# Kernel tuning notes

Measured on AMD Instinct MI355X. Metric: run time of the kernel, lower is better.

## Reference

```python
import jax, jax.numpy as jnp
import numpy as np

B, N = 8, 2048
D_MODEL, D_QK, NHEAD, N_K, D_FF = 256, 128, 8, 16, 1024
LN_EPS = 1e-5


def _layer_norm(x, g, b):
    m = jnp.mean(x, axis=-1, keepdims=True)
    v = jnp.var(x, axis=-1, keepdims=True)
    return (x - m) * jax.lax.rsqrt(v + LN_EPS) * g + b


def _l2_normalize(x):
    # F.normalize(dim=-1): x / max(||x||_2, 1e-12)
    n = jnp.sqrt(jnp.sum(x * x, axis=-1, keepdims=True))
    return x / jnp.maximum(n, 1e-12)


def setup_inputs() -> dict:
    key = jax.random.key(0)
    ks = jax.random.split(key, 12)
    s = 0.02
    return {
        "x": jax.random.normal(ks[0], (B, N, D_MODEL), dtype=jnp.float32),
        # linear_q / linear_k (d_model -> d_model_qk)
        "Wq": jax.random.normal(ks[1], (D_MODEL, D_QK), dtype=jnp.float32) * s,
        "bq": jnp.zeros((D_QK,), jnp.float32),
        "Wk": jax.random.normal(ks[2], (D_MODEL, D_QK), dtype=jnp.float32) * s,
        "bk": jnp.zeros((D_QK,), jnp.float32),
        # NoLinearQKMHA: value + output projections (d_model -> d_model)
        "Wv": jax.random.normal(ks[3], (D_MODEL, D_MODEL), dtype=jnp.float32) * s,
        "bv": jnp.zeros((D_MODEL,), jnp.float32),
        "Wo": jax.random.normal(ks[4], (D_MODEL, D_MODEL), dtype=jnp.float32) * s,
        "bo": jnp.zeros((D_MODEL,), jnp.float32),
        # norm1 (applied to gathered values)
        "g1": jnp.ones((D_MODEL,), jnp.float32),
        "b1": jnp.zeros((D_MODEL,), jnp.float32),
        # ffn: LayerNorm -> Linear -> GELU -> Linear
        "gf": jnp.ones((D_MODEL,), jnp.float32),
        "bf": jnp.zeros((D_MODEL,), jnp.float32),
        "W1": jax.random.normal(ks[5], (D_MODEL, D_FF), dtype=jnp.float32) * s,
        "b1f": jnp.zeros((D_FF,), jnp.float32),
        "W2": jax.random.normal(ks[6], (D_FF, D_MODEL), dtype=jnp.float32) * s,
        "b2f": jnp.zeros((D_MODEL,), jnp.float32),
        # residual_weight (init 0 in torch; nonzero here for a meaningful baseline)
        "rw": jnp.full((1,), 0.5, jnp.float32),
    }


def reference(x, Wq, bq, Wk, bk, Wv, bv, Wo, bo, g1, b1, gf, bf, W1, b1f, W2, b2f, rw):
    # --- project + normalize queries/keys ---
    qn = _l2_normalize(x @ Wq + bq)   # [B,N,Dqk]
    kn = _l2_normalize(x @ Wk + bk)   # [B,N,Dqk]

    # --- KNN: k smallest Euclidean distances from each query to keys ---
    d2 = (jnp.sum(qn * qn, -1)[:, :, None]
          + jnp.sum(kn * kn, -1)[:, None, :]
          - 2.0 * jnp.einsum('bqd,bkd->bqk', qn, kn))   # [B,N,N]
    _, idx = jax.lax.top_k(-d2, N_K)                     # [B,N,n_k]

    # --- gather neighbors ---
    gather = jax.vmap(lambda arr, ind: arr[ind])
    x_v = gather(x, idx)    # [B,N,n_k,D_MODEL]
    x_k = gather(kn, idx)   # [B,N,n_k,Dqk]

    # --- windowed MHA (NoLinearQK: q,k used directly; v projected) ---
    xnorm = _layer_norm(x_v, g1, b1)
    v = xnorm @ Wv + bv                                  # [B,N,n_k,D_MODEL]
    dh, dv = D_QK // NHEAD, D_MODEL // NHEAD
    qh = qn.reshape(B, N, NHEAD, dh)
    kh = x_k.reshape(B, N, N_K, NHEAD, dh)
    vh = v.reshape(B, N, N_K, NHEAD, dv)
    logits = jnp.einsum('bnhd,bnkhd->bnhk', qh, kh) / np.float32(np.sqrt(dh))
    attn = jax.nn.softmax(logits, axis=-1)
    o = jnp.einsum('bnhk,bnkhe->bnhe', attn, vh).reshape(B, N, D_MODEL)
    o = o @ Wo + bo

    # --- residuals (eval: dropout = identity) ---
    x = x + o * rw
    h = _layer_norm(x, gf, bf) @ W1 + b1f
    h = jax.nn.gelu(h, approximate=False) @ W2 + b2f
    x = x + h * rw
    return x
```

## Files before the change

### kernel.cpp

```cpp
#include <hip/hip_runtime.h>
#include <math.h>

#define BATCH 8
#define SEQ   2048
#define DM    256
#define DQK   128
#define NHEADS 8
#define NK    16
#define DFF   1024

typedef __attribute__((ext_vector_type(8))) short short8;
typedef __attribute__((ext_vector_type(8))) _Float16 half8;
typedef __attribute__((ext_vector_type(4))) float floatx4;
typedef unsigned long long ull;

__device__ __forceinline__ unsigned short f2bf(float f) {
    unsigned int u = __float_as_uint(f);
    u += 0x7fffu + ((u >> 16) & 1u);
    return (unsigned short)(u >> 16);
}

__device__ __forceinline__ float gelu_fast(float h) {
    float y = 0.7978845608028654f * (h + 0.044715f * h * h * h);
    float e = __expf(2.f * y);
    float t = 1.f - 2.f / (e + 1.f);
    return 0.5f * h * (1.f + t);
}

__device__ __forceinline__ ull mkkey(float f, int gidx) {
    unsigned int u = __float_as_uint(f);
    u ^= (unsigned int)((int)u >> 31) | 0x80000000u;
    return ((ull)u << 32) | (unsigned int)(2047 - gidx);
}

__device__ __forceinline__ ull shfl_xor_u64(ull v, int m) {
    unsigned int lo = (unsigned int)v, hi = (unsigned int)(v >> 32);
    lo = __shfl_xor(lo, m);
    hi = __shfl_xor(hi, m);
    return ((ull)hi << 32) | lo;
}

__global__ __launch_bounds__(256) void conv_kernel(
    const float* __restrict__ W1, const float* __restrict__ W2,
    const float* __restrict__ Wv, const float* __restrict__ Wo,
    unsigned short* __restrict__ W1f, unsigned short* __restrict__ W2f,
    unsigned short* __restrict__ Wvf, unsigned short* __restrict__ Wof)
{
    int g = blockIdx.x * 256 + threadIdx.x;
    const float* W; unsigned short* O; int e, stride;
    if (g < 32768)      { W = W1; O = W1f; e = g;         stride = DFF; }
    else if (g < 65536) { W = W2; O = W2f; e = g - 32768; stride = DM;  }
    else if (g < 73728) { W = Wv; O = Wvf; e = g - 65536; stride = DM;  }
    else                { W = Wo; O = Wof; e = g - 73728; stride = DM;  }
    int lane = e & 63;
    int kk, nt;
    if (g < 32768)      { kk = (e >> 6) & 7;  nt = e >> 9;  }
    else if (g < 65536) { kk = (e >> 6) & 31; nt = e >> 11; }
    else                { kk = (e >> 6) & 7;  nt = e >> 9;  }
    int n = nt * 16 + (lane & 15);
    int k0 = kk * 32 + (lane >> 4) * 8;
    unsigned int pk[4];
    #pragma unroll
    for (int jj = 0; jj < 4; ++jj) {
        unsigned short lo = f2bf(W[(size_t)(k0 + 2 * jj) * stride + n]);
        unsigned short hi = f2bf(W[(size_t)(k0 + 2 * jj + 1) * stride + n]);
        pk[jj] = (unsigned int)lo | ((unsigned int)hi << 16);
    }
    *(uint4*)(O + (size_t)e * 8) = make_uint4(pk[0], pk[1], pk[2], pk[3]);
}

__global__ __launch_bounds__(256) void proj_qk_kernel(
    const float* __restrict__ x,
    const float* __restrict__ Wq, const float* __restrict__ bq,
    const float* __restrict__ Wk, const float* __restrict__ bk,
    float* __restrict__ qn, float* __restrict__ kn,
    unsigned short* __restrict__ knTh, unsigned short* __restrict__ knTl,
    float* __restrict__ knsq)
{
    __shared__ __align__(16) float xs[8 * 256];
    __shared__ __align__(16) float ks[8 * 128];
    __shared__ float nred[8][2], kred[8][2], k2red[8][2];

    const int tid = threadIdx.x;
    const int b = blockIdx.x & 7;
    const int chunk = blockIdx.x >> 3;
    const size_t t0 = (size_t)b * SEQ + (size_t)chunk * 8;

    for (int i = tid; i < 8 * 256; i += 256) xs[i] = x[t0 * DM + i];
    __syncthreads();

    {
        const int col = tid & 127, half = tid >> 7;
        float qa[4] = {0.f, 0.f, 0.f, 0.f}, ka[4] = {0.f, 0.f, 0.f, 0.f};
        for (int d = 0; d < 256; ++d) {
            float wq = Wq[d * DQK + col];
            float wk = Wk[d * DQK + col];
            #pragma unroll
            for (int t = 0; t < 4; ++t) {
                float xv = xs[(half * 4 + t) * 256 + d];
                qa[t] = fmaf(xv, wq, qa[t]);
                ka[t] = fmaf(xv, wk, ka[t]);
            }
        }
        #pragma unroll
        for (int t = 0; t < 4; ++t) { qa[t] += bq[col]; ka[t] += bk[col]; }

        const int sub = (tid >> 6) & 1;
        #pragma unroll
        for (int t = 0; t < 4; ++t) {
            float sq = qa[t] * qa[t], sk = ka[t] * ka[t];
            #pragma unroll
            for (int m = 1; m < 64; m <<= 1) { sq += __shfl_xor(sq, m); sk += __shfl_xor(sk, m); }
            if ((tid & 63) == 0) { nred[half * 4 + t][sub] = sq; kred[half * 4 + t][sub] = sk; }
        }
        __syncthreads();
        float kvv[4];
        #pragma unroll
        for (int t = 0; t < 4; ++t) {
            int tok = half * 4 + t;
            float nq = sqrtf(nred[tok][0] + nred[tok][1]);
            float nk = sqrtf(kred[tok][0] + kred[tok][1]);
            float qv = qa[t] / fmaxf(nq, 1e-12f);
            float kv = ka[t] / fmaxf(nk, 1e-12f);
            qn[(t0 + tok) * DQK + col] = qv;
            kn[(t0 + tok) * DQK + col] = kv;
            ks[tok * 128 + col] = kv;
            kvv[t] = kv;
        }
        #pragma unroll
        for (int t = 0; t < 4; ++t) {
            float s2 = kvv[t] * kvv[t];
            #pragma unroll
            for (int m = 1; m < 64; m <<= 1) s2 += __shfl_xor(s2, m);
            if ((tid & 63) == 0) k2red[half * 4 + t][sub] = s2;
        }
        __syncthreads();
        if (tid < 8) knsq[t0 + tid] = k2red[tid][0] + k2red[tid][1];
    }

    {
        const int e   = tid & 127;
        const int sel = tid >> 7;
        const int key = e & 7;
        const int kq  = e >> 3;
        const int kk  = kq >> 2, qd = kq & 3;
        const int nt  = chunk >> 1;
        const int n   = ((chunk & 1) << 3) + key;
        const float* src = &ks[key * 128 + kk * 32 + qd * 8];
        unsigned int pk[4];
        #pragma unroll
        for (int jj = 0; jj < 4; ++jj) {
            float v0 = src[2 * jj], v1 = src[2 * jj + 1];
            _Float16 h0 = (_Float16)v0, h1 = (_Float16)v1;
            unsigned short u0, u1;
            if (sel == 0) {
                u0 = __builtin_bit_cast(unsigned short, h0);
                u1 = __builtin_bit_cast(unsigned short, h1);
            } else {
                _Float16 l0 = (_Float16)((v0 - (float)h0) * 4096.f);
                _Float16 l1 = (_Float16)((v1 - (float)h1) * 4096.f);
                u0 = __builtin_bit_cast(unsigned short, l0);
                u1 = __builtin_bit_cast(unsigned short, l1);
            }
            pk[jj] = (unsigned int)u0 | ((unsigned int)u1 << 16);
        }
        unsigned short* dst = (sel ? knTl : knTh)
            + (size_t)b * 262144
            + (size_t)((nt * 4 + kk) * 64 + qd * 16 + n) * 8;
        *(uint4*)dst = make_uint4(pk[0], pk[1], pk[2], pk[3]);
    }
}

__global__ __launch_bounds__(256) void proj_v_kernel(
    const float* __restrict__ x,
    const float* __restrict__ bv, const float* __restrict__ g1,
    const float* __restrict__ b1,
    const unsigned short* __restrict__ Wvf, float* __restrict__ vall)
{
    __shared__ __align__(16) float xs[16][260];
    __shared__ float stat_m[16], stat_r[16];
    __shared__ float bvs[256], g1s[256], b1s[256];

    const int tid = threadIdx.x;
    const int lane = tid & 63, wave = tid >> 6;
    const int quad = lane >> 4, lr = lane & 15;
    const size_t t0 = (size_t)blockIdx.x * 16;

    for (int i = tid; i < 16 * 256; i += 256) xs[i >> 8][i & 255] = x[t0 * DM + i];
    bvs[tid] = bv[tid]; g1s[tid] = g1[tid]; b1s[tid] = b1[tid];
    __syncthreads();

    {
        int tok = tid >> 4, l = tid & 15;
        float s = 0.f, s2 = 0.f;
        #pragma unroll
        for (int i = 0; i < 16; ++i) {
            float v = xs[tok][l + 16 * i];
            s += v; s2 += v * v;
        }
        #pragma unroll
        for (int m = 1; m < 16; m <<= 1) { s += __shfl_xor(s, m); s2 += __shfl_xor(s2, m); }
        if (l == 0) {
            float mean = s * (1.f / 256.f);
            float var  = s2 * (1.f / 256.f) - mean * mean;
            stat_m[tok] = mean;
            stat_r[tok] = rsqrtf(var + 1e-5f);
        }
    }
    __syncthreads();

    short8 av[8];
    {
        float mm = stat_m[lr], rr = stat_r[lr];
        #pragma unroll
        for (int kk = 0; kk < 8; ++kk) {
            #pragma unroll
            for (int j = 0; j < 8; ++j) {
                int k = kk * 32 + quad * 8 + j;
                float v = (xs[lr][k] - mm) * rr * g1s[k] + b1s[k];
                av[kk][j] = (short)f2bf(v);
            }
        }
    }
    floatx4 acc[4];
    #pragma unroll
    for (int nt = 0; nt < 4; ++nt) acc[nt] = (floatx4){0.f, 0.f, 0.f, 0.f};
    #pragma unroll
    for (int nt = 0; nt < 4; ++nt) {
        #pragma unroll
        for (int kk = 0; kk < 8; ++kk) {
            short8 bfr = *(const short8*)(Wvf + ((size_t)(((wave * 4 + nt) * 8 + kk) * 64) + lane) * 8);
            acc[nt] = __builtin_amdgcn_mfma_f32_16x16x32_bf16(av[kk], bfr, acc[nt], 0, 0, 0);
        }
    }
    #pragma unroll
    for (int nt = 0; nt < 4; ++nt) {
        int col = (wave * 4 + nt) * 16 + lr;
        float bb = bvs[col];
        #pragma unroll
        for (int reg = 0; reg < 4; ++reg) {
            int row = quad * 4 + reg;
            vall[(t0 + row) * DM + col] = acc[nt][reg] + bb;
        }
    }
}

__global__ __launch_bounds__(256, 4) void attn_kernel(
    const float* __restrict__ x,
    const float* __restrict__ qn_g, const float* __restrict__ kn_g,
    const unsigned short* __restrict__ knTh, const unsigned short* __restrict__ knTl,
    const float* __restrict__ knsq_g,
    const float* __restrict__ vall,
    const unsigned short* __restrict__ Wof, const float* __restrict__ bo,
    const float* __restrict__ rw, float* __restrict__ out)
{
    __shared__ __align__(16) float s_ld[8 * 1024];
    __shared__ __align__(16) float qs[8 * DQK];
    __shared__ ull candK[8][32];
    __shared__ int topidx[8 * NK];
    float* attn_s = s_ld;
    float* o8     = s_ld + 1024;

    const int tid = threadIdx.x;
    const int lane = tid & 63, wave = tid >> 6;
    const int quad = lane >> 4, lr = lane & 15;
    const int sg = lane >> 5, sl = lane & 31;
    const int qsel = wave * 2 + sg;
    const int b = blockIdx.x & 7;
    const int chunk = blockIdx.x >> 3;
    const size_t tq0 = (size_t)b * SEQ + (size_t)chunk * 8;
    const size_t rowb = (size_t)b * SEQ;

    *(float4*)&qs[tid * 4] = *(const float4*)&qn_g[tq0 * DQK + tid * 4];

    half8 a_hi[4], a_lo[4];
    {
        const float* qrow = qn_g + (tq0 + (lr & 7)) * DQK + quad * 8;
        #pragma unroll
        for (int kk = 0; kk < 4; ++kk) {
            float4 fa = *(const float4*)(qrow + kk * 32);
            float4 fb = *(const float4*)(qrow + kk * 32 + 4);
            float vv[8] = {fa.x, fa.y, fa.z, fa.w, fb.x, fb.y, fb.z, fb.w};
            #pragma unroll
            for (int j = 0; j < 8; ++j) {
                float v = vv[j];
                _Float16 h = (_Float16)v;
                a_hi[kk][j] = h;
                a_lo[kk][j] = (_Float16)((v - (float)h) * 4096.f);
            }
        }
    }
    __syncthreads();

    const unsigned short* bh = knTh + (size_t)b * 262144;
    const unsigned short* bl = knTl + (size_t)b * 262144;
    const float* ksqb = knsq_g + rowb;

    for (int h = 0; h < 2; ++h) {
        if (h) __syncthreads();

        for (int t = 0; t < 16; ++t) {
            const int tile = h * 64 + wave * 16 + t;
            const unsigned short* ph = bh + (size_t)tile * 2048 + lane * 8;
            const unsigned short* pl = bl + (size_t)tile * 2048 + lane * 8;
            floatx4 am  = (floatx4){0.f, 0.f, 0.f, 0.f};
            floatx4 ax1 = (floatx4){0.f, 0.f, 0.f, 0.f};
            floatx4 ax2 = (floatx4){0.f, 0.f, 0.f, 0.f};
            #pragma unroll
            for (int kk = 0; kk < 4; ++kk) {
                half8 bhf = *(const half8*)(ph + kk * 512);
                half8 blf = *(const half8*)(pl + kk * 512);
                am  = __builtin_amdgcn_mfma_f32_16x16x32_f16(a_hi[kk], bhf, am,  0, 0, 0);
                ax1 = __builtin_amdgcn_mfma_f32_16x16x32_f16(a_hi[kk], blf, ax1, 0, 0, 0);
                ax2 = __builtin_amdgcn_mfma_f32_16x16x32_f16(a_lo[kk], bhf, ax2, 0, 0, 0);
            }
            if (lane < 32) {
                const int keyloc = (wave * 16 + t) * 16 + lr;
                const float kq = ksqb[h * 1024 + keyloc];
                #pragma unroll
                for (int r = 0; r < 4; ++r) {
                    s_ld[(quad * 4 + r) * 1024 + keyloc] =
                        2.f * (am[r] + (ax1[r] + ax2[r]) * (1.f / 4096.f)) - kq;
                }
            }
        }
        __syncthreads();

        {
            const float* srow = &s_ld[qsel * 1024 + sl];
            float f0 = -INFINITY, f1 = -INFINITY;
            int   i0 = 0, i1 = 0;
            #pragma unroll
            for (int i = 0; i < 32; ++i) {
                float f = srow[32 * i];
                int gidx = h * 1024 + sl + 32 * i;
                bool a  = f > f0;
                bool bb = f > f1;
                f1 = a ? f0 : (bb ? f    : f1);
                i1 = a ? i0 : (bb ? gidx : i1);
                f0 = a ? f    : f0;
                i0 = a ? gidx : i0;
            }
            ull k2v = mkkey(f1, i1);
            ull cur = mkkey(f0, i0);
            int cnt = 0;
            for (int r = 0; r < NK; ++r) {
                ull w = cur;
                #pragma unroll
                for (int m = 1; m < 32; m <<= 1) {
                    ull o = shfl_xor_u64(w, m);
                    if (o > w) w = o;
                }
                if (sl == 0) candK[qsel][h * 16 + r] = w;
                if (cur == w) {
                    ++cnt;
                    if (cnt == 1) cur = k2v;
                    else {
                        ull best = 0;
                        #pragma unroll
                        for (int i = 0; i < 32; ++i) {
                            float f = srow[32 * i];
                            ull k = mkkey(f, h * 1024 + sl + 32 * i);
                            if (k < w && k > best) best = k;
                        }
                        cur = best;
                    }
                }
            }
        }
    }
    __syncthreads();

    {
        ull cur = candK[qsel][sl];
        for (int r = 0; r < NK; ++r) {
            ull w = cur;
            #pragma unroll
            for (int m = 1; m < 32; m <<= 1) {
                ull o = shfl_xor_u64(w, m);
                if (o > w) w = o;
            }
            if (sl == 0) topidx[qsel * NK + r] = 2047 - (int)(unsigned int)(w & 0xFFFFFFFFull);
            if (cur == w) cur = 0;
        }
    }
    __syncthreads();

    for (int qq = 0; qq < 2; ++qq) {
        const int q = wave + 4 * qq;
        const int h = lane >> 3;
        const int k1 = lane & 7, k2 = 8 + (lane & 7);
        const int i1 = topidx[q * NK + k1], i2 = topidx[q * NK + k2];
        const float* kr1 = kn_g + (rowb + i1) * DQK + h * 16;
        const float* kr2 = kn_g + (rowb + i2) * DQK + h * 16;
        float lg1 = 0.f, lg2 = 0.f;
        #pragma unroll
        for (int d = 0; d < 16; d += 4) {
            float4 qv = *(const float4*)&qs[q * DQK + h * 16 + d];
            float4 a1 = *(const float4*)&kr1[d];
            float4 a2 = *(const float4*)&kr2[d];
            lg1 = fmaf(qv.x, a1.x, lg1); lg1 = fmaf(qv.y, a1.y, lg1);
            lg1 = fmaf(qv.z, a1.z, lg1); lg1 = fmaf(qv.w, a1.w, lg1);
            lg2 = fmaf(qv.x, a2.x, lg2); lg2 = fmaf(qv.y, a2.y, lg2);
            lg2 = fmaf(qv.z, a2.z, lg2); lg2 = fmaf(qv.w, a2.w, lg2);
        }
        lg1 *= 0.25f; lg2 *= 0.25f;
        float mx = fmaxf(lg1, lg2);
        #pragma unroll
        for (int m = 1; m < 8; m <<= 1) mx = fmaxf(mx, __shfl_xor(mx, m));
        float e1 = expf(lg1 - mx), e2 = expf(lg2 - mx);
        float ssum = e1 + e2;
        #pragma unroll
        for (int m = 1; m < 8; m <<= 1) ssum += __shfl_xor(ssum, m);
        attn_s[q * 128 + h * 16 + k1] = e1 / ssum;
        attn_s[q * 128 + h * 16 + k2] = e2 / ssum;
        __syncthreads();

        float o[4] = {0.f, 0.f, 0.f, 0.f};
        for (int k = 0; k < NK; ++k) {
            const float* vr = vall + (rowb + topidx[q * NK + k]) * DM;
            #pragma unroll
            for (int j = 0; j < 4; ++j) {
                int d = lane + 64 * j;
                o[j] = fmaf(attn_s[q * 128 + (d >> 5) * 16 + k], vr[d], o[j]);
            }
        }
        #pragma unroll
        for (int j = 0; j < 4; ++j) o8[q * 260 + lane + 64 * j] = o[j];
        __syncthreads();
    }

    {
        short8 ao[8];
        #pragma unroll
        for (int kk = 0; kk < 8; ++kk) {
            #pragma unroll
            for (int j = 0; j < 8; ++j) {
                int k = kk * 32 + quad * 8 + j;
                float v = (lr < 8) ? o8[lr * 260 + k] : 0.f;
                ao[kk][j] = (short)f2bf(v);
            }
        }
        floatx4 aw[4];
        #pragma unroll
        for (int nt = 0; nt < 4; ++nt) aw[nt] = (floatx4){0.f, 0.f, 0.f, 0.f};
        #pragma unroll
        for (int nt = 0; nt < 4; ++nt) {
            #pragma unroll
            for (int kk = 0; kk < 8; ++kk) {
                short8 bofr = *(const short8*)(Wof + ((size_t)(((wave * 4 + nt) * 8 + kk) * 64) + lane) * 8);
                aw[nt] = __builtin_amdgcn_mfma_f32_16x16x32_bf16(ao[kk], bofr, aw[nt], 0, 0, 0);
            }
        }
        float rwv = rw[0];
        if (quad < 2) {
            #pragma unroll
            for (int nt = 0; nt < 4; ++nt) {
                int col = (wave * 4 + nt) * 16 + lr;
                float bov = bo[col];
                #pragma unroll
                for (int reg = 0; reg < 4; ++reg) {
                    int row = quad * 4 + reg;
                    size_t t = tq0 + row;
                    out[t * DM + col] = x[t * DM + col] + (aw[nt][reg] + bov) * rwv;
                }
            }
        }
    }
}

__global__ __launch_bounds__(256, 2) void ffn_kernel(
    float* __restrict__ io,
    const float* __restrict__ gf, const float* __restrict__ bf,
    const unsigned short* __restrict__ W1f, const float* __restrict__ b1f,
    const unsigned short* __restrict__ W2f, const float* __restrict__ b2f,
    const float* __restrict__ rw)
{
    __shared__ __align__(16) float xs[16][260];
    __shared__ float gfs[256], bfs[256], b2s[256], b1s[1024];
    __shared__ float stat_m[16], stat_r[16];
    __shared__ __align__(16) unsigned short Af[8 * 64 * 8];
    __shared__ __align__(16) unsigned short G[16][1032];

    const int tid = threadIdx.x;
    const int lane = tid & 63, wave = tid >> 6;
    const int quad = lane >> 4, lr = lane & 15;
    const size_t t0 = (size_t)blockIdx.x * 16;

    for (int i = tid; i < 16 * 256; i += 256) xs[i >> 8][i & 255] = io[t0 * DM + i];
    gfs[tid] = gf[tid]; bfs[tid] = bf[tid]; b2s[tid] = b2f[tid];
    for (int i = tid; i < 1024; i += 256) b1s[i] = b1f[i];
    __syncthreads();

    {
        int tok = tid >> 4, l = tid & 15;
        float s = 0.f, s2 = 0.f;
        #pragma unroll
        for (int i = 0; i < 16; ++i) {
            float v = xs[tok][l + 16 * i];
            s += v; s2 += v * v;
        }
        #pragma unroll
        for (int m = 1; m < 16; m <<= 1) { s += __shfl_xor(s, m); s2 += __shfl_xor(s2, m); }
        if (l == 0) {
            float mean = s * (1.f / 256.f);
            float var  = s2 * (1.f / 256.f) - mean * mean;
            stat_m[tok] = mean;
            stat_r[tok] = rsqrtf(var + 1e-5f);
        }
    }
    __syncthreads();

    for (int kk = wave; kk < 8; kk += 4) {
        int m = lr, k0 = kk * 32 + quad * 8;
        float mm = stat_m[m], rr = stat_r[m];
        unsigned int pk[4];
        #pragma unroll
        for (int jj = 0; jj < 4; ++jj) {
            int ka = k0 + 2 * jj, kb = ka + 1;
            float v0 = (xs[m][ka] - mm) * rr * gfs[ka] + bfs[ka];
            float v1 = (xs[m][kb] - mm) * rr * gfs[kb] + bfs[kb];
            pk[jj] = (unsigned int)f2bf(v0) | ((unsigned int)f2bf(v1) << 16);
        }
        *(uint4*)&Af[(kk * 64 + lane) * 8] = make_uint4(pk[0], pk[1], pk[2], pk[3]);
    }
    __syncthreads();

    short8 afr[8];
    #pragma unroll
    for (int kk = 0; kk < 8; ++kk)
        afr[kk] = *(const short8*)&Af[(kk * 64 + lane) * 8];

    floatx4 acc[16];
    #pragma unroll
    for (int nt = 0; nt < 16; ++nt) acc[nt] = (floatx4){0.f, 0.f, 0.f, 0.f};

    const unsigned short* w1p = W1f + ((size_t)(wave * 16) * 8 * 64) * 8;
    for (int nt = 0; nt < 16; ++nt) {
        #pragma unroll
        for (int kk = 0; kk < 8; ++kk) {
            short8 bfr = *(const short8*)(w1p + (size_t)((nt * 8 + kk) * 64 + lane) * 8);
            acc[nt] = __builtin_amdgcn_mfma_f32_16x16x32_bf16(afr[kk], bfr, acc[nt], 0, 0, 0);
        }
    }

    #pragma unroll
    for (int nt = 0; nt < 16; ++nt) {
        #pragma unroll
        for (int reg = 0; reg < 4; ++reg) {
            int n = wave * 256 + nt * 16 + lr;
            int row = quad * 4 + reg;
            float h = acc[nt][reg] + b1s[n];
            G[row][n] = f2bf(gelu_fast(h));
        }
    }
    __syncthreads();

    floatx4 acc2[4];
    #pragma unroll
    for (int nt = 0; nt < 4; ++nt) acc2[nt] = (floatx4){0.f, 0.f, 0.f, 0.f};

    for (int kk2 = 0; kk2 < 32; ++kk2) {
        short8 a2 = *(const short8*)&G[lr][kk2 * 32 + quad * 8];
        #pragma unroll
        for (int nt = 0; nt < 4; ++nt) {
            short8 b2 = *(const short8*)(W2f + (size_t)(((wave * 4 + nt) * 32 + kk2) * 64 + lane) * 8);
            acc2[nt] = __builtin_amdgcn_mfma_f32_16x16x32_bf16(a2, b2, acc2[nt], 0, 0, 0);
        }
    }

    float rwv = rw[0];
    #pragma unroll
    for (int nt = 0; nt < 4; ++nt) {
        #pragma unroll
        for (int reg = 0; reg < 4; ++reg) {
            int col = wave * 64 + nt * 16 + lr;
            int row = quad * 4 + reg;
            float o = acc2[nt][reg] + b2s[col];
            io[(t0 + row) * DM + col] = xs[row][col] + o * rwv;
        }
    }
}

extern "C" void kernel_launch(void* const* d_in, const int* in_sizes, int n_in,
                              void* d_out, int out_size, void* d_ws, size_t ws_size,
                              hipStream_t stream)
{
    const float* x   = (const float*)d_in[0];
    const float* Wq  = (const float*)d_in[1];
    const float* bq  = (const float*)d_in[2];
    const float* Wk  = (const float*)d_in[3];
    const float* bk  = (const float*)d_in[4];
    const float* Wv  = (const float*)d_in[5];
    const float* bv  = (const float*)d_in[6];
    const float* Wo  = (const float*)d_in[7];
    const float* bo  = (const float*)d_in[8];
    const float* g1  = (const float*)d_in[9];
    const float* b1  = (const float*)d_in[10];
    const float* gf  = (const float*)d_in[11];
    const float* bf  = (const float*)d_in[12];
    const float* W1  = (const float*)d_in[13];
    const float* b1f = (const float*)d_in[14];
    const float* W2  = (const float*)d_in[15];
    const float* b2f = (const float*)d_in[16];
    const float* rw  = (const float*)d_in[17];
    float* out = (float*)d_out;

    float* ws   = (float*)d_ws;
    float* qn   = ws;
    float* kn   = ws + 2097152;
    unsigned short* knTh = (unsigned short*)(ws + 4194304);
    unsigned short* knTl = knTh + 2097152;
    float* vall = ws + 6291456;
    float* knsq = ws + 10485760;
    unsigned short* W1f = (unsigned short*)(ws + 10502144);
    unsigned short* W2f = W1f + 262144;
    unsigned short* Wvf = W2f + 262144;
    unsigned short* Wof = Wvf + 65536;

    conv_kernel<<<320, 256, 0, stream>>>(W1, W2, Wv, Wo, W1f, W2f, Wvf, Wof);
    proj_qk_kernel<<<BATCH * SEQ / 8, 256, 0, stream>>>(x, Wq, bq, Wk, bk,
                                                        qn, kn, knTh, knTl, knsq);
    proj_v_kernel<<<BATCH * SEQ / 16, 256, 0, stream>>>(x, bv, g1, b1, Wvf, vall);
    attn_kernel<<<BATCH * SEQ / 8, 256, 0, stream>>>(x, qn, kn, knTh, knTl, knsq, vall,
                                                     Wof, bo, rw, out);
    ffn_kernel<<<BATCH * SEQ / 16, 256, 0, stream>>>(out, gf, bf, W1f, b1f, W2f, b2f, rw);
}
```

Before: 381.3 us.

## Process 16 queries per attention block and 32 tokens per FFN block

The attention kernel now handles 16 queries per block instead of 8. This fills all 16 MFMA rows, which were previously half wasted, so each key tile read from memory serves twice as many queries. The top-k stage is restructured into four key quarters with candidates held in registers, and the final merge uses the two candidates per lane. The FFN kernel moves to 512 threads and 32 tokens per block so each W1/W2 fragment feeds two row tiles. The cost is fewer blocks, more LDS per block, and higher register pressure.

```diff
diff --git a/kernel.cpp b/kernel.cpp
--- a/kernel.cpp
+++ b/kernel.cpp
@@ -254,28 +254,24 @@
     const unsigned short* __restrict__ Wof, const float* __restrict__ bo,
     const float* __restrict__ rw, float* __restrict__ out)
 {
-    __shared__ __align__(16) float s_ld[8 * 1024];
-    __shared__ __align__(16) float qs[8 * DQK];
-    __shared__ ull candK[8][32];
-    __shared__ int topidx[8 * NK];
+    __shared__ __align__(16) float s_ld[16 * 512];
+    __shared__ int topidx[16 * NK];
     float* attn_s = s_ld;
-    float* o8     = s_ld + 1024;
+    float* o8     = s_ld + 2048;
 
     const int tid = threadIdx.x;
     const int lane = tid & 63, wave = tid >> 6;
     const int quad = lane >> 4, lr = lane & 15;
     const int sg = lane >> 5, sl = lane & 31;
-    const int qsel = wave * 2 + sg;
+    const int sgid = wave * 2 + sg;
     const int b = blockIdx.x & 7;
     const int chunk = blockIdx.x >> 3;
-    const size_t tq0 = (size_t)b * SEQ + (size_t)chunk * 8;
+    const size_t tq0 = (size_t)b * SEQ + (size_t)chunk * 16;
     const size_t rowb = (size_t)b * SEQ;
 
-    *(float4*)&qs[tid * 4] = *(const float4*)&qn_g[tq0 * DQK + tid * 4];
-
     half8 a_hi[4], a_lo[4];
     {
-        const float* qrow = qn_g + (tq0 + (lr & 7)) * DQK + quad * 8;
+        const float* qrow = qn_g + (tq0 + lr) * DQK + quad * 8;
         #pragma unroll
         for (int kk = 0; kk < 4; ++kk) {
             float4 fa = *(const float4*)(qrow + kk * 32);
@@ -290,17 +286,18 @@
             }
         }
     }
-    __syncthreads();
 
     const unsigned short* bh = knTh + (size_t)b * 262144;
     const unsigned short* bl = knTl + (size_t)b * 262144;
     const float* ksqb = knsq_g + rowb;
 
-    for (int h = 0; h < 2; ++h) {
-        if (h) __syncthreads();
-
-        for (int t = 0; t < 16; ++t) {
-            const int tile = h * 64 + wave * 16 + t;
+    ull c0[2], c1[2];
+
+    for (int q4 = 0; q4 < 4; ++q4) {
+        if (q4) __syncthreads();
+
+        for (int t = 0; t < 8; ++t) {
+            const int tile = q4 * 32 + wave * 8 + t;
             const unsigned short* ph = bh + (size_t)tile * 2048 + lane * 8;
             const unsigned short* pl = bl + (size_t)tile * 2048 + lane * 8;
             floatx4 am  = (floatx4){0.f, 0.f, 0.f, 0.f};
@@ -314,26 +311,26 @@
                 ax1 = __builtin_amdgcn_mfma_f32_16x16x32_f16(a_hi[kk], blf, ax1, 0, 0, 0);
                 ax2 = __builtin_amdgcn_mfma_f32_16x16x32_f16(a_lo[kk], bhf, ax2, 0, 0, 0);
             }
-            if (lane < 32) {
-                const int keyloc = (wave * 16 + t) * 16 + lr;
-                const float kq = ksqb[h * 1024 + keyloc];
-                #pragma unroll
-                for (int r = 0; r < 4; ++r) {
-                    s_ld[(quad * 4 + r) * 1024 + keyloc] =
-                        2.f * (am[r] + (ax1[r] + ax2[r]) * (1.f / 4096.f)) - kq;
-                }
+            const int keyloc = (wave * 8 + t) * 16 + lr;
+            const float kq = ksqb[q4 * 512 + keyloc];
+            #pragma unroll
+            for (int r = 0; r < 4; ++r) {
+                s_ld[(quad * 4 + r) * 512 + keyloc] =
+                    2.f * (am[r] + (ax1[r] + ax2[r]) * (1.f / 4096.f)) - kq;
             }
         }
         __syncthreads();
 
-        {
-            const float* srow = &s_ld[qsel * 1024 + sl];
+        #pragma unroll
+        for (int qi = 0; qi < 2; ++qi) {
+            const int q = sgid + 8 * qi;
+            const float* srow = &s_ld[q * 512 + sl];
             float f0 = -INFINITY, f1 = -INFINITY;
             int   i0 = 0, i1 = 0;
             #pragma unroll
-            for (int i = 0; i < 32; ++i) {
+            for (int i = 0; i < 16; ++i) {
                 float f = srow[32 * i];
-                int gidx = h * 1024 + sl + 32 * i;
+                int gidx = q4 * 512 + sl + 32 * i;
                 bool a  = f > f0;
                 bool bb = f > f1;
                 f1 = a ? f0 : (bb ? f    : f1);
@@ -351,16 +348,18 @@
                     ull o = shfl_xor_u64(w, m);
                     if (o > w) w = o;
                 }
-                if (sl == 0) candK[qsel][h * 16 + r] = w;
+                const int slot = q4 * 16 + r;
+                if (sl == slot)      c0[qi] = w;
+                if (sl == slot - 32) c1[qi] = w;
                 if (cur == w) {
                     ++cnt;
                     if (cnt == 1) cur = k2v;
                     else {
                         ull best = 0;
                         #pragma unroll
-                        for (int i = 0; i < 32; ++i) {
+                        for (int i = 0; i < 16; ++i) {
                             float f = srow[32 * i];
-                            ull k = mkkey(f, h * 1024 + sl + 32 * i);
+                            ull k = mkkey(f, q4 * 512 + sl + 32 * i);
                             if (k < w && k > best) best = k;
                         }
                         cur = best;
@@ -371,8 +370,14 @@
     }
     __syncthreads();
 
-    {
-        ull cur = candK[qsel][sl];
+    #pragma unroll
+    for (int qi = 0; qi < 2; ++qi) {
+        const int q = sgid + 8 * qi;
+        ull ca = c0[qi], cb = c1[qi];
+        ull hi = ca > cb ? ca : cb;
+        ull lo = ca > cb ? cb : ca;
+        ull cur = hi;
+        int cnt = 0;
         for (int r = 0; r < NK; ++r) {
             ull w = cur;
             #pragma unroll
@@ -380,23 +385,24 @@
                 ull o = shfl_xor_u64(w, m);
                 if (o > w) w = o;
             }
-            if (sl == 0) topidx[qsel * NK + r] = 2047 - (int)(unsigned int)(w & 0xFFFFFFFFull);
-            if (cur == w) cur = 0;
-        }
-    }
-    __syncthreads();
-
-    for (int qq = 0; qq < 2; ++qq) {
+            if (sl == 0) topidx[q * NK + r] = 2047 - (int)(unsigned int)(w & 0xFFFFFFFFull);
+            if (cur == w) { ++cnt; cur = (cnt == 1) ? lo : 0ull; }
+        }
+    }
+    __syncthreads();
+
+    for (int qq = 0; qq < 4; ++qq) {
         const int q = wave + 4 * qq;
         const int h = lane >> 3;
         const int k1 = lane & 7, k2 = 8 + (lane & 7);
         const int i1 = topidx[q * NK + k1], i2 = topidx[q * NK + k2];
+        const float* qrow = qn_g + (tq0 + q) * DQK + h * 16;
         const float* kr1 = kn_g + (rowb + i1) * DQK + h * 16;
         const float* kr2 = kn_g + (rowb + i2) * DQK + h * 16;
         float lg1 = 0.f, lg2 = 0.f;
         #pragma unroll
         for (int d = 0; d < 16; d += 4) {
-            float4 qv = *(const float4*)&qs[q * DQK + h * 16 + d];
+            float4 qv = *(const float4*)&qrow[d];
             float4 a1 = *(const float4*)&kr1[d];
             float4 a2 = *(const float4*)&kr2[d];
             lg1 = fmaf(qv.x, a1.x, lg1); lg1 = fmaf(qv.y, a1.y, lg1);
@@ -437,8 +443,7 @@
             #pragma unroll
             for (int j = 0; j < 8; ++j) {
                 int k = kk * 32 + quad * 8 + j;
-                float v = (lr < 8) ? o8[lr * 260 + k] : 0.f;
-                ao[kk][j] = (short)f2bf(v);
+                ao[kk][j] = (short)f2bf(o8[lr * 260 + k]);
             }
         }
         floatx4 aw[4];
@@ -453,43 +458,41 @@
             }
         }
         float rwv = rw[0];
-        if (quad < 2) {
-            #pragma unroll
-            for (int nt = 0; nt < 4; ++nt) {
-                int col = (wave * 4 + nt) * 16 + lr;
-                float bov = bo[col];
-                #pragma unroll
-                for (int reg = 0; reg < 4; ++reg) {
-                    int row = quad * 4 + reg;
-                    size_t t = tq0 + row;
-                    out[t * DM + col] = x[t * DM + col] + (aw[nt][reg] + bov) * rwv;
-                }
-            }
-        }
-    }
-}
-
-__global__ __launch_bounds__(256, 2) void ffn_kernel(
+        #pragma unroll
+        for (int nt = 0; nt < 4; ++nt) {
+            int col = (wave * 4 + nt) * 16 + lr;
+            float bov = bo[col];
+            #pragma unroll
+            for (int reg = 0; reg < 4; ++reg) {
+                int row = quad * 4 + reg;
+                size_t t = tq0 + row;
+                out[t * DM + col] = x[t * DM + col] + (aw[nt][reg] + bov) * rwv;
+            }
+        }
+    }
+}
+
+__global__ __launch_bounds__(512, 1) void ffn_kernel(
     float* __restrict__ io,
     const float* __restrict__ gf, const float* __restrict__ bf,
     const unsigned short* __restrict__ W1f, const float* __restrict__ b1f,
     const unsigned short* __restrict__ W2f, const float* __restrict__ b2f,
     const float* __restrict__ rw)
 {
-    __shared__ __align__(16) float xs[16][260];
+    __shared__ __align__(16) float xs[32][260];
     __shared__ float gfs[256], bfs[256], b2s[256], b1s[1024];
-    __shared__ float stat_m[16], stat_r[16];
-    __shared__ __align__(16) unsigned short Af[8 * 64 * 8];
-    __shared__ __align__(16) unsigned short G[16][1032];
+    __shared__ float stat_m[32], stat_r[32];
+    __shared__ __align__(16) unsigned short Af[2][8 * 64 * 8];
+    __shared__ __align__(16) unsigned short G[32][1032];
 
     const int tid = threadIdx.x;
     const int lane = tid & 63, wave = tid >> 6;
     const int quad = lane >> 4, lr = lane & 15;
-    const size_t t0 = (size_t)blockIdx.x * 16;
-
-    for (int i = tid; i < 16 * 256; i += 256) xs[i >> 8][i & 255] = io[t0 * DM + i];
-    gfs[tid] = gf[tid]; bfs[tid] = bf[tid]; b2s[tid] = b2f[tid];
-    for (int i = tid; i < 1024; i += 256) b1s[i] = b1f[i];
+    const size_t t0 = (size_t)blockIdx.x * 32;
+
+    for (int i = tid; i < 32 * 256; i += 512) xs[i >> 8][i & 255] = io[t0 * DM + i];
+    if (tid < 256) { gfs[tid] = gf[tid]; bfs[tid] = bf[tid]; b2s[tid] = b2f[tid]; }
+    for (int i = tid; i < 1024; i += 512) b1s[i] = b1f[i];
     __syncthreads();
 
     {
@@ -511,73 +514,83 @@
     }
     __syncthreads();
 
-    for (int kk = wave; kk < 8; kk += 4) {
-        int m = lr, k0 = kk * 32 + quad * 8;
-        float mm = stat_m[m], rr = stat_r[m];
-        unsigned int pk[4];
-        #pragma unroll
-        for (int jj = 0; jj < 4; ++jj) {
-            int ka = k0 + 2 * jj, kb = ka + 1;
-            float v0 = (xs[m][ka] - mm) * rr * gfs[ka] + bfs[ka];
-            float v1 = (xs[m][kb] - mm) * rr * gfs[kb] + bfs[kb];
-            pk[jj] = (unsigned int)f2bf(v0) | ((unsigned int)f2bf(v1) << 16);
-        }
-        *(uint4*)&Af[(kk * 64 + lane) * 8] = make_uint4(pk[0], pk[1], pk[2], pk[3]);
-    }
-    __syncthreads();
-
-    short8 afr[8];
-    #pragma unroll
-    for (int kk = 0; kk < 8; ++kk)
-        afr[kk] = *(const short8*)&Af[(kk * 64 + lane) * 8];
-
-    floatx4 acc[16];
-    #pragma unroll
-    for (int nt = 0; nt < 16; ++nt) acc[nt] = (floatx4){0.f, 0.f, 0.f, 0.f};
-
-    const unsigned short* w1p = W1f + ((size_t)(wave * 16) * 8 * 64) * 8;
-    for (int nt = 0; nt < 16; ++nt) {
+    {
+        const int rt = wave >> 2;
+        for (int kk = wave & 3; kk < 8; kk += 4) {
+            int m = rt * 16 + lr, k0 = kk * 32 + quad * 8;
+            float mm = stat_m[m], rr = stat_r[m];
+            unsigned int pk[4];
+            #pragma unroll
+            for (int jj = 0; jj < 4; ++jj) {
+                int ka = k0 + 2 * jj, kb = ka + 1;
+                float v0 = (xs[m][ka] - mm) * rr * gfs[ka] + bfs[ka];
+                float v1 = (xs[m][kb] - mm) * rr * gfs[kb] + bfs[kb];
+                pk[jj] = (unsigned int)f2bf(v0) | ((unsigned int)f2bf(v1) << 16);
+            }
+            *(uint4*)&Af[rt][(kk * 64 + lane) * 8] = make_uint4(pk[0], pk[1], pk[2], pk[3]);
+        }
+    }
+    __syncthreads();
+
+    short8 afr[2][8];
+    #pragma unroll
+    for (int rt = 0; rt < 2; ++rt)
+        #pragma unroll
+        for (int kk = 0; kk < 8; ++kk)
+            afr[rt][kk] = *(const short8*)&Af[rt][(kk * 64 + lane) * 8];
+
+    for (int nt = 0; nt < 8; ++nt) {
+        floatx4 acc0 = (floatx4){0.f, 0.f, 0.f, 0.f};
+        floatx4 acc1 = (floatx4){0.f, 0.f, 0.f, 0.f};
+        const int ntg = wave * 8 + nt;
         #pragma unroll
         for (int kk = 0; kk < 8; ++kk) {
-            short8 bfr = *(const short8*)(w1p + (size_t)((nt * 8 + kk) * 64 + lane) * 8);
-            acc[nt] = __builtin_amdgcn_mfma_f32_16x16x32_bf16(afr[kk], bfr, acc[nt], 0, 0, 0);
-        }
-    }
-
-    #pragma unroll
-    for (int nt = 0; nt < 16; ++nt) {
+            short8 bfr = *(const short8*)(W1f + (size_t)((ntg * 8 + kk) * 64 + lane) * 8);
+            acc0 = __builtin_amdgcn_mfma_f32_16x16x32_bf16(afr[0][kk], bfr, acc0, 0, 0, 0);
+            acc1 = __builtin_amdgcn_mfma_f32_16x16x32_bf16(afr[1][kk], bfr, acc1, 0, 0, 0);
+        }
+        const int n = ntg * 16 + lr;
+        const float bb = b1s[n];
         #pragma unroll
         for (int reg = 0; reg < 4; ++reg) {
-            int n = wave * 256 + nt * 16 + lr;
             int row = quad * 4 + reg;
-            float h = acc[nt][reg] + b1s[n];
-            G[row][n] = f2bf(gelu_fast(h));
-        }
-    }
-    __syncthreads();
-
-    floatx4 acc2[4];
-    #pragma unroll
-    for (int nt = 0; nt < 4; ++nt) acc2[nt] = (floatx4){0.f, 0.f, 0.f, 0.f};
+            G[row][n]      = f2bf(gelu_fast(acc0[reg] + bb));
+            G[row + 16][n] = f2bf(gelu_fast(acc1[reg] + bb));
+        }
+    }
+    __syncthreads();
+
+    floatx4 acc2[2][2];
+    #pragma unroll
+    for (int nt2 = 0; nt2 < 2; ++nt2)
+        #pragma unroll
+        for (int rt = 0; rt < 2; ++rt)
+            acc2[nt2][rt] = (floatx4){0.f, 0.f, 0.f, 0.f};
 
     for (int kk2 = 0; kk2 < 32; ++kk2) {
-        short8 a2 = *(const short8*)&G[lr][kk2 * 32 + quad * 8];
-        #pragma unroll
-        for (int nt = 0; nt < 4; ++nt) {
-            short8 b2 = *(const short8*)(W2f + (size_t)(((wave * 4 + nt) * 32 + kk2) * 64 + lane) * 8);
-            acc2[nt] = __builtin_amdgcn_mfma_f32_16x16x32_bf16(a2, b2, acc2[nt], 0, 0, 0);
+        short8 a20 = *(const short8*)&G[lr][kk2 * 32 + quad * 8];
+        short8 a21 = *(const short8*)&G[16 + lr][kk2 * 32 + quad * 8];
+        #pragma unroll
+        for (int nt2 = 0; nt2 < 2; ++nt2) {
+            short8 b2 = *(const short8*)(W2f + (size_t)((((wave * 2 + nt2) * 32 + kk2) * 64 + lane) * 8));
+            acc2[nt2][0] = __builtin_amdgcn_mfma_f32_16x16x32_bf16(a20, b2, acc2[nt2][0], 0, 0, 0);
+            acc2[nt2][1] = __builtin_amdgcn_mfma_f32_16x16x32_bf16(a21, b2, acc2[nt2][1], 0, 0, 0);
         }
     }
 
     float rwv = rw[0];
     #pragma unroll
-    for (int nt = 0; nt < 4; ++nt) {
-        #pragma unroll
-        for (int reg = 0; reg < 4; ++reg) {
-            int col = wave * 64 + nt * 16 + lr;
-            int row = quad * 4 + reg;
-            float o = acc2[nt][reg] + b2s[col];
-            io[(t0 + row) * DM + col] = xs[row][col] + o * rwv;
+    for (int nt2 = 0; nt2 < 2; ++nt2) {
+        int col = (wave * 2 + nt2) * 16 + lr;
+        float bb = b2s[col];
+        #pragma unroll
+        for (int rt = 0; rt < 2; ++rt) {
+            #pragma unroll
+            for (int reg = 0; reg < 4; ++reg) {
+                int row = rt * 16 + quad * 4 + reg;
+                float o = acc2[nt2][rt][reg] + bb;
+                io[(t0 + row) * DM + col] = xs[row][col] + o * rwv;
+            }
         }
     }
 }
@@ -622,7 +635,7 @@
     proj_qk_kernel<<<BATCH * SEQ / 8, 256, 0, stream>>>(x, Wq, bq, Wk, bk,
                                                         qn, kn, knTh, knTl, knsq);
     proj_v_kernel<<<BATCH * SEQ / 16, 256, 0, stream>>>(x, bv, g1, b1, Wvf, vall);
-    attn_kernel<<<BATCH * SEQ / 8, 256, 0, stream>>>(x, qn, kn, knTh, knTl, knsq, vall,
-                                                     Wof, bo, rw, out);
-    ffn_kernel<<<BATCH * SEQ / 16, 256, 0, stream>>>(out, gf, bf, W1f, b1f, W2f, b2f, rw);
-}
+    attn_kernel<<<BATCH * SEQ / 16, 256, 0, stream>>>(x, qn, kn, knTh, knTl, knsq, vall,
+                                                      Wof, bo, rw, out);
+    ffn_kernel<<<BATCH * SEQ / 32, 512, 0, stream>>>(out, gf, bf, W1f, b1f, W2f, b2f, rw);
+}
```

Result: faster. 350.0 us (-8.2%).
